# Kernel optimization log

Measured on AMD Instinct MI355X. Metric: run time of the kernel, lower is better.

## Reference

```python
import jax, jax.numpy as jnp
import numpy as np

B, S, D_IN, D_OUT = 4, 8192, 1024, 1024


def setup_inputs() -> dict:
    key = jax.random.key(0)
    k1, k2, k3, k4 = jax.random.split(key, 4)
    x = jax.random.normal(k1, (B, S, D_IN), dtype=jnp.float32)
    # signed int8 weights, stored int8 as in the torch buffer
    weight_int = jax.random.randint(k2, (D_OUT, D_IN), -128, 128, dtype=jnp.int32).astype(jnp.int8)
    # realistic per-output-channel scales
    weight_scale = jax.random.uniform(k3, (D_OUT,), dtype=jnp.float32, minval=0.005, maxval=0.02)
    input_scale = jnp.asarray(0.05, dtype=jnp.float32)
    bias = jax.random.normal(k4, (D_OUT,), dtype=jnp.float32) * 0.01
    return {"x": x, "weight_int": weight_int, "weight_scale": weight_scale,
            "input_scale": input_scale, "bias": bias}


def reference(x, weight_int, weight_scale, input_scale, bias):
    # quantize activations to int8 (faithful: round, clamp, cast)
    x_int = jnp.clip(jnp.round(x / input_scale), -128, 127).astype(jnp.int8)
    # module upcasts both operands to fp32 for the matmul
    out = jnp.matmul(x_int.astype(jnp.float32), weight_int.astype(jnp.float32).T)
    # dequantize: per-output-channel weight scale * scalar input scale, then bias
    out = out * weight_scale * input_scale + bias
    return out
```

## Files before the change

### kernel.cpp

```cpp
#include <hip/hip_runtime.h>
#include <stdint.h>
#include <stddef.h>

typedef int   v4i __attribute__((ext_vector_type(4)));
typedef float v4f __attribute__((ext_vector_type(4)));

#define BM 128
#define BN 128
#define BKB 128
#define M_DIM 32768
#define N_DIM 1024
#define K_DIM 1024

typedef const __attribute__((address_space(1))) void gvoid_t;
typedef __attribute__((address_space(3))) void lvoid_t;

__device__ __forceinline__ void gload16(const void* g, void* l) {
    __builtin_amdgcn_global_load_lds((gvoid_t*)g, (lvoid_t*)l, 16, 0, 0);
}

__global__ __launch_bounds__(256)
void repack_w_kernel(const int* __restrict__ wi, int* __restrict__ wq, int n4)
{
    int i = blockIdx.x * blockDim.x + threadIdx.x;
    if (i < n4) {
        v4i v = ((const v4i*)wi)[i];
        wq[i] = (v[0] & 255) | ((v[1] & 255) << 8) |
                ((v[2] & 255) << 16) | ((v[3] & 255) << 24);
    }
}

__global__ __launch_bounds__(256, 2)
void quant_kernel(const float* __restrict__ x, int* __restrict__ q,
                  const float* __restrict__ iscale_p, int n4)
{
    const float is = *iscale_p;
    int idx = blockIdx.x * blockDim.x + threadIdx.x;
    int stride = gridDim.x * blockDim.x;
    const v4f* xp = (const v4f*)x;
    for (int i = idx; i < n4; i += stride) {
        v4f v = xp[i];
        int r = 0;
        #pragma unroll
        for (int j = 0; j < 4; ++j) {
            float t = rintf(v[j] / is);
            t = fminf(127.f, fmaxf(-128.f, t));
            r |= ((int)t & 255) << (8 * j);
        }
        q[i] = r;
    }
}

__global__ __launch_bounds__(256, 2)
void qgemm_kernel(const signed char* __restrict__ Aq,
                  const signed char* __restrict__ W,
                  const float* __restrict__ wscale,
                  const float* __restrict__ iscale_p,
                  const float* __restrict__ bias,
                  float* __restrict__ out)
{
    __shared__ signed char lA[BM * BKB];
    __shared__ signed char lB[BN * BKB];

    const int nwg = gridDim.x;
    const int bid = blockIdx.x;
    const int wg  = (bid & 7) * (nwg >> 3) + (bid >> 3);
    const int m_blk = wg >> 3;
    const int n_blk = wg & 7;
    const int mrow0 = m_blk * BM;
    const int ncol0 = n_blk * BN;

    const int tid = threadIdx.x;
    const int wv  = tid >> 6;
    const int ln  = tid & 63;
    const int wm  = wv >> 1;
    const int wn  = wv & 1;
    const int lrow = ln & 15;
    const int lk16 = (ln >> 4) << 4;
    const int swz  = (lrow & 7) << 4;

    v4i acc[4][4] = {};

    for (int kt = 0; kt < K_DIM; kt += BKB) {
        __syncthreads();
        #pragma unroll
        for (int c = 0; c < 4; ++c) {
            const int o   = c * 4096 + wv * 1024 + ln * 16;
            const int row = o >> 7;
            const int inr = (o & 127) ^ ((row & 7) << 4);
            gload16(Aq + (size_t)(mrow0 + row) * K_DIM + kt + inr,
                    (void*)(lA + c * 4096 + wv * 1024));
            gload16(W + (size_t)(ncol0 + row) * K_DIM + kt + inr,
                    (void*)(lB + c * 4096 + wv * 1024));
        }
        __syncthreads();
        #pragma unroll
        for (int st = 0; st < 2; ++st) {
            v4i af[4], bf[4];
            #pragma unroll
            for (int i = 0; i < 4; ++i) {
                const int arow = wm * 64 + i * 16 + lrow;
                af[i] = *(const v4i*)&lA[arow * BKB + ((st * 64 + lk16) ^ swz)];
                const int brow = wn * 64 + i * 16 + lrow;
                bf[i] = *(const v4i*)&lB[brow * BKB + ((st * 64 + lk16) ^ swz)];
            }
            #pragma unroll
            for (int i = 0; i < 4; ++i)
                #pragma unroll
                for (int j = 0; j < 4; ++j)
                    acc[i][j] = __builtin_amdgcn_mfma_i32_16x16x64_i8(
                                    af[i], bf[j], acc[i][j], 0, 0, 0);
        }
    }

    const float is = *iscale_p;
    const int r0 = mrow0 + wm * 64 + ((ln >> 4) << 2);
    const int c0 = ncol0 + wn * 64 + lrow;
    #pragma unroll
    for (int j = 0; j < 4; ++j) {
        const int col = c0 + j * 16;
        const float sc = wscale[col] * is;
        const float bv = bias[col];
        #pragma unroll
        for (int i = 0; i < 4; ++i) {
            const int row = r0 + i * 16;
            #pragma unroll
            for (int r = 0; r < 4; ++r)
                out[(size_t)(row + r) * N_DIM + col] = (float)acc[i][j][r] * sc + bv;
        }
    }
}

extern "C" void kernel_launch(void* const* d_in, const int* in_sizes, int n_in,
                              void* d_out, int out_size, void* d_ws, size_t ws_size,
                              hipStream_t stream)
{
    const float* x       = (const float*)d_in[0];
    const int*   w32     = (const int*)d_in[1];
    const float* wscale  = (const float*)d_in[2];
    const float* iscale  = (const float*)d_in[3];
    const float* bias    = (const float*)d_in[4];
    float* out           = (float*)d_out;

    signed char* aq = (signed char*)d_ws;
    signed char* wq = (signed char*)d_ws + (size_t)M_DIM * K_DIM;

    const int wn4 = (N_DIM * K_DIM) / 4;
    repack_w_kernel<<<(wn4 + 255) / 256, 256, 0, stream>>>(w32, (int*)wq, wn4);

    quant_kernel<<<8192, 256, 0, stream>>>(x, (int*)aq, iscale, (M_DIM * K_DIM) / 4);

    const int grid = (M_DIM / BM) * (N_DIM / BN);
    qgemm_kernel<<<grid, 256, 0, stream>>>(aq, wq, wscale, iscale, bias, out);
}
```

Before: 85.49 us.

## Use 256x256 tiles with double-buffered LDS and interleaved load/MFMA pipeline

Rewrites the int8 GEMM to use 256x256 output tiles with 512 threads and double-buffered LDS. Global-to-LDS loads for the next K tile are split into quarters and interleaved between four MFMA phases, coordinated with explicit vmcnt waits, barriers and setprio. This raises arithmetic intensity and hides load latency, at the cost of more LDS (128KB) and more registers per thread, which may limit occupancy. The quantization kernel also replaces its per-element division with a multiply by a precomputed reciprocal, which can change rounding in rare cases.

```diff
diff --git a/kernel.cpp b/kernel.cpp
--- a/kernel.cpp
+++ b/kernel.cpp
@@ -5,12 +5,13 @@
 typedef int   v4i __attribute__((ext_vector_type(4)));
 typedef float v4f __attribute__((ext_vector_type(4)));
 
-#define BM 128
-#define BN 128
-#define BKB 128
 #define M_DIM 32768
 #define N_DIM 1024
 #define K_DIM 1024
+#define BM 256
+#define BN 256
+#define BK 128
+#define NT (K_DIM / BK)
 
 typedef const __attribute__((address_space(1))) void gvoid_t;
 typedef __attribute__((address_space(3))) void lvoid_t;
@@ -18,6 +19,10 @@
 __device__ __forceinline__ void gload16(const void* g, void* l) {
     __builtin_amdgcn_global_load_lds((gvoid_t*)g, (lvoid_t*)l, 16, 0, 0);
 }
+
+#define VMCNT(n)  asm volatile("s_waitcnt vmcnt(" #n ")" ::: "memory")
+#define BARRIER() do { asm volatile("s_barrier" ::: "memory"); \
+                       __builtin_amdgcn_sched_barrier(0); } while (0)
 
 __global__ __launch_bounds__(256)
 void repack_w_kernel(const int* __restrict__ wi, int* __restrict__ wq, int n4)
@@ -34,7 +39,7 @@
 void quant_kernel(const float* __restrict__ x, int* __restrict__ q,
                   const float* __restrict__ iscale_p, int n4)
 {
-    const float is = *iscale_p;
+    const float inv = 1.0f / *iscale_p;
     int idx = blockIdx.x * blockDim.x + threadIdx.x;
     int stride = gridDim.x * blockDim.x;
     const v4f* xp = (const v4f*)x;
@@ -43,7 +48,7 @@
         int r = 0;
         #pragma unroll
         for (int j = 0; j < 4; ++j) {
-            float t = rintf(v[j] / is);
+            float t = rintf(v[j] * inv);
             t = fminf(127.f, fmaxf(-128.f, t));
             r |= ((int)t & 255) << (8 * j);
         }
@@ -51,7 +56,35 @@
     }
 }
 
-__global__ __launch_bounds__(256, 2)
+__device__ __forceinline__ void stageA(const signed char* __restrict__ gA,
+                                       signed char* ldsA, int q, int wv, int ln)
+{
+    #pragma unroll
+    for (int l = 0; l < 2; ++l) {
+        const int r0  = l * 128 + q * 64 + wv * 8;
+        const int row = r0 + (ln >> 3);
+        const int col = ((ln & 7) * 16) ^ ((ln >> 3) << 4);
+        gload16(gA + (size_t)row * K_DIM + col, ldsA + r0 * BK);
+    }
+}
+__device__ __forceinline__ void stageB(const signed char* __restrict__ gB,
+                                       signed char* ldsB, int q, int wv, int ln)
+{
+    #pragma unroll
+    for (int l = 0; l < 2; ++l) {
+        const int r0  = (2 * l + (wv >> 2)) * 64 + q * 32 + (wv & 3) * 8;
+        const int row = r0 + (ln >> 3);
+        const int col = ((ln & 7) * 16) ^ ((ln >> 3) << 4);
+        gload16(gB + (size_t)row * K_DIM + col, ldsB + r0 * BK);
+    }
+}
+
+__device__ __forceinline__ v4i ldsRead(const signed char* lds, int row, int colb)
+{
+    return *(const v4i*)(lds + row * BK + (colb ^ ((row & 7) << 4)));
+}
+
+__global__ __launch_bounds__(512, 2)
 void qgemm_kernel(const signed char* __restrict__ Aq,
                   const signed char* __restrict__ W,
                   const float* __restrict__ wscale,
@@ -59,74 +92,137 @@
                   const float* __restrict__ bias,
                   float* __restrict__ out)
 {
-    __shared__ signed char lA[BM * BKB];
-    __shared__ signed char lB[BN * BKB];
-
-    const int nwg = gridDim.x;
+    __shared__ signed char lA[2][BM * BK];
+    __shared__ signed char lB[2][BN * BK];
+
     const int bid = blockIdx.x;
-    const int wg  = (bid & 7) * (nwg >> 3) + (bid >> 3);
-    const int m_blk = wg >> 3;
-    const int n_blk = wg & 7;
+    const int wg  = (bid & 7) * 64 + (bid >> 3);
+    const int m_blk = wg >> 2;
+    const int n_blk = wg & 3;
     const int mrow0 = m_blk * BM;
     const int ncol0 = n_blk * BN;
 
     const int tid = threadIdx.x;
     const int wv  = tid >> 6;
     const int ln  = tid & 63;
-    const int wm  = wv >> 1;
-    const int wn  = wv & 1;
-    const int lrow = ln & 15;
-    const int lk16 = (ln >> 4) << 4;
-    const int swz  = (lrow & 7) << 4;
-
-    v4i acc[4][4] = {};
-
-    for (int kt = 0; kt < K_DIM; kt += BKB) {
-        __syncthreads();
-        #pragma unroll
-        for (int c = 0; c < 4; ++c) {
-            const int o   = c * 4096 + wv * 1024 + ln * 16;
-            const int row = o >> 7;
-            const int inr = (o & 127) ^ ((row & 7) << 4);
-            gload16(Aq + (size_t)(mrow0 + row) * K_DIM + kt + inr,
-                    (void*)(lA + c * 4096 + wv * 1024));
-            gload16(W + (size_t)(ncol0 + row) * K_DIM + kt + inr,
-                    (void*)(lB + c * 4096 + wv * 1024));
-        }
-        __syncthreads();
-        #pragma unroll
-        for (int st = 0; st < 2; ++st) {
-            v4i af[4], bf[4];
-            #pragma unroll
-            for (int i = 0; i < 4; ++i) {
-                const int arow = wm * 64 + i * 16 + lrow;
-                af[i] = *(const v4i*)&lA[arow * BKB + ((st * 64 + lk16) ^ swz)];
-                const int brow = wn * 64 + i * 16 + lrow;
-                bf[i] = *(const v4i*)&lB[brow * BKB + ((st * 64 + lk16) ^ swz)];
-            }
-            #pragma unroll
-            for (int i = 0; i < 4; ++i)
-                #pragma unroll
-                for (int j = 0; j < 4; ++j)
-                    acc[i][j] = __builtin_amdgcn_mfma_i32_16x16x64_i8(
-                                    af[i], bf[j], acc[i][j], 0, 0, 0);
-        }
+    const int wm  = wv >> 2;
+    const int wn  = wv & 3;
+    const int lr  = ln & 15;
+    const int kc  = (ln >> 4) * 16;
+
+    const signed char* gA = Aq + (size_t)mrow0 * K_DIM;
+    const signed char* gB = W  + (size_t)ncol0 * K_DIM;
+
+    v4i acc[8][4] = {};
+    v4i aF[4][2];
+    v4i bF[2][2][2];
+
+    stageA(gA, lA[0], 0, wv, ln);
+    stageB(gB, lB[0], 0, wv, ln);
+    stageB(gB, lB[0], 1, wv, ln);
+    stageA(gA, lA[0], 1, wv, ln);
+
+    #pragma unroll
+    for (int t = 0; t < NT; ++t) {
+        const signed char* cA = lA[t & 1];
+        const signed char* cB = lB[t & 1];
+        signed char* nA = lA[(t + 1) & 1];
+        signed char* nB = lB[(t + 1) & 1];
+        const size_t ktn = (size_t)(t + 1) * BK;
+        const bool st = (t + 1 < NT);
+
+        VMCNT(4);
+        BARRIER();
+        #pragma unroll
+        for (int m = 0; m < 4; ++m)
+            #pragma unroll
+            for (int ks = 0; ks < 2; ++ks)
+                aF[m][ks] = ldsRead(cA, wm * 128 + m * 16 + lr, ks * 64 + kc);
+        #pragma unroll
+        for (int n = 0; n < 2; ++n)
+            #pragma unroll
+            for (int ks = 0; ks < 2; ++ks)
+                bF[0][n][ks] = ldsRead(cB, wn * 64 + n * 16 + lr, ks * 64 + kc);
+        if (st) stageA(gA + ktn, nA, 0, wv, ln);
+        BARRIER();
+        __builtin_amdgcn_s_setprio(1);
+        #pragma unroll
+        for (int m = 0; m < 4; ++m)
+            #pragma unroll
+            for (int n = 0; n < 2; ++n)
+                #pragma unroll
+                for (int ks = 0; ks < 2; ++ks)
+                    acc[m][n] = __builtin_amdgcn_mfma_i32_16x16x64_i8(
+                                    aF[m][ks], bF[0][n][ks], acc[m][n], 0, 0, 0);
+        __builtin_amdgcn_s_setprio(0);
+
+        if (st) { VMCNT(4); } else { VMCNT(2); }
+        BARRIER();
+        #pragma unroll
+        for (int n = 0; n < 2; ++n)
+            #pragma unroll
+            for (int ks = 0; ks < 2; ++ks)
+                bF[1][n][ks] = ldsRead(cB, wn * 64 + 32 + n * 16 + lr, ks * 64 + kc);
+        if (st) stageB(gB + ktn, nB, 0, wv, ln);
+        BARRIER();
+        __builtin_amdgcn_s_setprio(1);
+        #pragma unroll
+        for (int m = 0; m < 4; ++m)
+            #pragma unroll
+            for (int n = 0; n < 2; ++n)
+                #pragma unroll
+                for (int ks = 0; ks < 2; ++ks)
+                    acc[m][2 + n] = __builtin_amdgcn_mfma_i32_16x16x64_i8(
+                                    aF[m][ks], bF[1][n][ks], acc[m][2 + n], 0, 0, 0);
+        __builtin_amdgcn_s_setprio(0);
+
+        if (st) { VMCNT(4); } else { VMCNT(0); }
+        BARRIER();
+        #pragma unroll
+        for (int m = 0; m < 4; ++m)
+            #pragma unroll
+            for (int ks = 0; ks < 2; ++ks)
+                aF[m][ks] = ldsRead(cA, wm * 128 + 64 + m * 16 + lr, ks * 64 + kc);
+        if (st) stageB(gB + ktn, nB, 1, wv, ln);
+        BARRIER();
+        __builtin_amdgcn_s_setprio(1);
+        #pragma unroll
+        for (int m = 0; m < 4; ++m)
+            #pragma unroll
+            for (int n = 0; n < 2; ++n)
+                #pragma unroll
+                for (int ks = 0; ks < 2; ++ks)
+                    acc[4 + m][2 + n] = __builtin_amdgcn_mfma_i32_16x16x64_i8(
+                                    aF[m][ks], bF[1][n][ks], acc[4 + m][2 + n], 0, 0, 0);
+        __builtin_amdgcn_s_setprio(0);
+
+        BARRIER();
+        if (st) stageA(gA + ktn, nA, 1, wv, ln);
+        BARRIER();
+        __builtin_amdgcn_s_setprio(1);
+        #pragma unroll
+        for (int m = 0; m < 4; ++m)
+            #pragma unroll
+            for (int n = 0; n < 2; ++n)
+                #pragma unroll
+                for (int ks = 0; ks < 2; ++ks)
+                    acc[4 + m][n] = __builtin_amdgcn_mfma_i32_16x16x64_i8(
+                                    aF[m][ks], bF[0][n][ks], acc[4 + m][n], 0, 0, 0);
+        __builtin_amdgcn_s_setprio(0);
     }
 
     const float is = *iscale_p;
-    const int r0 = mrow0 + wm * 64 + ((ln >> 4) << 2);
-    const int c0 = ncol0 + wn * 64 + lrow;
-    #pragma unroll
-    for (int j = 0; j < 4; ++j) {
-        const int col = c0 + j * 16;
+    #pragma unroll
+    for (int n = 0; n < 4; ++n) {
+        const int col = ncol0 + wn * 64 + n * 16 + lr;
         const float sc = wscale[col] * is;
         const float bv = bias[col];
         #pragma unroll
-        for (int i = 0; i < 4; ++i) {
-            const int row = r0 + i * 16;
+        for (int m = 0; m < 8; ++m) {
+            const int row = mrow0 + wm * 128 + m * 16 + ((ln >> 4) << 2);
             #pragma unroll
             for (int r = 0; r < 4; ++r)
-                out[(size_t)(row + r) * N_DIM + col] = (float)acc[i][j][r] * sc + bv;
+                out[(size_t)(row + r) * N_DIM + col] = (float)acc[m][n][r] * sc + bv;
         }
     }
 }
@@ -151,5 +247,5 @@
     quant_kernel<<<8192, 256, 0, stream>>>(x, (int*)aq, iscale, (M_DIM * K_DIM) / 4);
 
     const int grid = (M_DIM / BM) * (N_DIM / BN);
-    qgemm_kernel<<<grid, 256, 0, stream>>>(aq, wq, wscale, iscale, bias, out);
-}
+    qgemm_kernel<<<grid, 512, 0, stream>>>(aq, wq, wscale, iscale, bias, out);
+}
```

After: 91.08 us. 6.5% more time.

## Enlarge GEMM tiles to 256x256, double-buffer LDS, switch to 32x32x32 int8 MFMA

Applied to the files above, without the earlier changes.

The int8 GEMM now uses 256x256 output tiles with BK=64, giving each wave a 128x128 sub-tile built from 32x32x32 i8 MFMAs with 16-wide accumulators. The LDS stage is double-buffered so the next K-slice loads while the current one computes, with explicit vmcnt waits, raw barriers and setprio around the MFMA block. The quantizer also replaces a per-element divide with a multiply by a precomputed reciprocal, which can change rounding at ties relative to the reference. The larger accumulator footprint raises register pressure and lowers occupancy (launch bounds no longer request two blocks per CU).

```diff
diff --git a/kernel.cpp b/kernel.cpp
--- a/kernel.cpp
+++ b/kernel.cpp
@@ -2,15 +2,17 @@
 #include <stdint.h>
 #include <stddef.h>
 
-typedef int   v4i __attribute__((ext_vector_type(4)));
-typedef float v4f __attribute__((ext_vector_type(4)));
+typedef int   v4i  __attribute__((ext_vector_type(4)));
+typedef int   v16i __attribute__((ext_vector_type(16)));
+typedef float v4f  __attribute__((ext_vector_type(4)));
 
-#define BM 128
-#define BN 128
-#define BKB 128
 #define M_DIM 32768
 #define N_DIM 1024
 #define K_DIM 1024
+#define BM 256
+#define BN 256
+#define BK 64
+#define NT (K_DIM / BK)
 
 typedef const __attribute__((address_space(1))) void gvoid_t;
 typedef __attribute__((address_space(3))) void lvoid_t;
@@ -18,6 +20,10 @@
 __device__ __forceinline__ void gload16(const void* g, void* l) {
     __builtin_amdgcn_global_load_lds((gvoid_t*)g, (lvoid_t*)l, 16, 0, 0);
 }
+
+#define VMCNT0()  asm volatile("s_waitcnt vmcnt(0)" ::: "memory")
+#define BARRIER() do { asm volatile("s_barrier" ::: "memory"); \
+                       __builtin_amdgcn_sched_barrier(0); } while (0)
 
 __global__ __launch_bounds__(256)
 void repack_w_kernel(const int* __restrict__ wi, int* __restrict__ wq, int n4)
@@ -34,7 +40,7 @@
 void quant_kernel(const float* __restrict__ x, int* __restrict__ q,
                   const float* __restrict__ iscale_p, int n4)
 {
-    const float is = *iscale_p;
+    const float inv = 1.0f / *iscale_p;
     int idx = blockIdx.x * blockDim.x + threadIdx.x;
     int stride = gridDim.x * blockDim.x;
     const v4f* xp = (const v4f*)x;
@@ -43,7 +49,7 @@
         int r = 0;
         #pragma unroll
         for (int j = 0; j < 4; ++j) {
-            float t = rintf(v[j] / is);
+            float t = rintf(v[j] * inv);
             t = fminf(127.f, fmaxf(-128.f, t));
             r |= ((int)t & 255) << (8 * j);
         }
@@ -51,7 +57,26 @@
     }
 }
 
-__global__ __launch_bounds__(256, 2)
+__device__ __forceinline__ int swz(int row) { return ((row >> 1) & 3) << 4; }
+
+__device__ __forceinline__ void stage64(const signed char* __restrict__ g,
+                                        signed char* lds, int wv, int ln)
+{
+    #pragma unroll
+    for (int j = 0; j < 4; ++j) {
+        const int rbase = j * 64 + wv * 16;
+        const int row   = rbase + (ln >> 2);
+        const int src   = ((ln & 3) * 16) ^ swz(row);
+        gload16(g + (size_t)row * K_DIM + src, lds + rbase * BK);
+    }
+}
+
+__device__ __forceinline__ v4i frag(const signed char* lds, int row, int kb)
+{
+    return *(const v4i*)(lds + row * BK + (kb ^ swz(row)));
+}
+
+__global__ __launch_bounds__(256)
 void qgemm_kernel(const signed char* __restrict__ Aq,
                   const signed char* __restrict__ W,
                   const float* __restrict__ wscale,
@@ -59,14 +84,13 @@
                   const float* __restrict__ bias,
                   float* __restrict__ out)
 {
-    __shared__ signed char lA[BM * BKB];
-    __shared__ signed char lB[BN * BKB];
+    __shared__ signed char lA[2][BM * BK];
+    __shared__ signed char lB[2][BN * BK];
 
-    const int nwg = gridDim.x;
     const int bid = blockIdx.x;
-    const int wg  = (bid & 7) * (nwg >> 3) + (bid >> 3);
-    const int m_blk = wg >> 3;
-    const int n_blk = wg & 7;
+    const int wg  = (bid & 7) * 64 + (bid >> 3);
+    const int m_blk = wg >> 2;
+    const int n_blk = wg & 3;
     const int mrow0 = m_blk * BM;
     const int ncol0 = n_blk * BN;
 
@@ -75,58 +99,65 @@
     const int ln  = tid & 63;
     const int wm  = wv >> 1;
     const int wn  = wv & 1;
-    const int lrow = ln & 15;
-    const int lk16 = (ln >> 4) << 4;
-    const int swz  = (lrow & 7) << 4;
+    const int lr  = ln & 31;
+    const int kh  = (ln >> 5) * 16;
 
-    v4i acc[4][4] = {};
+    const signed char* gA = Aq + (size_t)mrow0 * K_DIM;
+    const signed char* gB = W  + (size_t)ncol0 * K_DIM;
 
-    for (int kt = 0; kt < K_DIM; kt += BKB) {
-        __syncthreads();
+    v16i acc[4][4] = {};
+
+    stage64(gA, lA[0], wv, ln);
+    stage64(gB, lB[0], wv, ln);
+    VMCNT0();
+    BARRIER();
+
+    signed char *cA = lA[0], *cB = lB[0], *nA = lA[1], *nB = lB[1];
+
+    for (int t = 0; t < NT; ++t) {
+        const bool st = (t + 1 < NT);
+        if (st) {
+            stage64(gA + (size_t)(t + 1) * BK, nA, wv, ln);
+            stage64(gB + (size_t)(t + 1) * BK, nB, wv, ln);
+        }
         #pragma unroll
-        for (int c = 0; c < 4; ++c) {
-            const int o   = c * 4096 + wv * 1024 + ln * 16;
-            const int row = o >> 7;
-            const int inr = (o & 127) ^ ((row & 7) << 4);
-            gload16(Aq + (size_t)(mrow0 + row) * K_DIM + kt + inr,
-                    (void*)(lA + c * 4096 + wv * 1024));
-            gload16(W + (size_t)(ncol0 + row) * K_DIM + kt + inr,
-                    (void*)(lB + c * 4096 + wv * 1024));
-        }
-        __syncthreads();
-        #pragma unroll
-        for (int st = 0; st < 2; ++st) {
-            v4i af[4], bf[4];
+        for (int ks = 0; ks < 2; ++ks) {
+            v4i aF[4], bF[4];
             #pragma unroll
             for (int i = 0; i < 4; ++i) {
-                const int arow = wm * 64 + i * 16 + lrow;
-                af[i] = *(const v4i*)&lA[arow * BKB + ((st * 64 + lk16) ^ swz)];
-                const int brow = wn * 64 + i * 16 + lrow;
-                bf[i] = *(const v4i*)&lB[brow * BKB + ((st * 64 + lk16) ^ swz)];
+                aF[i] = frag(cA, wm * 128 + i * 32 + lr, ks * 32 + kh);
+                bF[i] = frag(cB, wn * 128 + i * 32 + lr, ks * 32 + kh);
             }
+            __builtin_amdgcn_s_setprio(1);
             #pragma unroll
             for (int i = 0; i < 4; ++i)
                 #pragma unroll
                 for (int j = 0; j < 4; ++j)
-                    acc[i][j] = __builtin_amdgcn_mfma_i32_16x16x64_i8(
-                                    af[i], bf[j], acc[i][j], 0, 0, 0);
+                    acc[i][j] = __builtin_amdgcn_mfma_i32_32x32x32_i8(
+                                    aF[i], bF[j], acc[i][j], 0, 0, 0);
+            __builtin_amdgcn_s_setprio(0);
         }
+        if (st) VMCNT0();
+        BARRIER();
+        signed char* s;
+        s = cA; cA = nA; nA = s;
+        s = cB; cB = nB; nB = s;
     }
 
     const float is = *iscale_p;
-    const int r0 = mrow0 + wm * 64 + ((ln >> 4) << 2);
-    const int c0 = ncol0 + wn * 64 + lrow;
     #pragma unroll
     for (int j = 0; j < 4; ++j) {
-        const int col = c0 + j * 16;
+        const int col = ncol0 + wn * 128 + j * 32 + lr;
         const float sc = wscale[col] * is;
         const float bv = bias[col];
         #pragma unroll
         for (int i = 0; i < 4; ++i) {
-            const int row = r0 + i * 16;
+            const int rbase = mrow0 + wm * 128 + i * 32 + 4 * (ln >> 5);
             #pragma unroll
-            for (int r = 0; r < 4; ++r)
-                out[(size_t)(row + r) * N_DIM + col] = (float)acc[i][j][r] * sc + bv;
+            for (int r = 0; r < 16; ++r) {
+                const int row = rbase + (r & 3) + 8 * (r >> 2);
+                out[(size_t)row * N_DIM + col] = (float)acc[i][j][r] * sc + bv;
+            }
         }
     }
 }
```

New measurement: 105.3 us. 23.1% more time.

## Double-buffer LDS in int8 GEMM and fuse quantize with weight repack

Applied to the files above, without the earlier changes.

The GEMM main loop now uses two LDS buffers, so the global-to-LDS loads for the next K tile are issued before the MFMAs on the current tile. This replaces the two barriers per iteration with a single vmcnt wait plus barrier, and wraps the MFMA block in s_setprio. The activation quantize kernel and the weight repack kernel are merged into one launch by splitting on block index, removing one kernel launch. The quantize step now multiplies by a precomputed reciprocal instead of dividing. That could change rounding at exact .5 ties relative to the reference, and doubling LDS per block may lower occupancy.

```diff
diff --git a/kernel.cpp b/kernel.cpp
--- a/kernel.cpp
+++ b/kernel.cpp
@@ -11,6 +11,10 @@
 #define M_DIM 32768
 #define N_DIM 1024
 #define K_DIM 1024
+#define NT (K_DIM / BKB)
+#define QN4 (M_DIM * K_DIM / 4)
+#define WN4 (N_DIM * K_DIM / 4)
+#define QBLOCKS 8192
 
 typedef const __attribute__((address_space(1))) void gvoid_t;
 typedef __attribute__((address_space(3))) void lvoid_t;
@@ -19,35 +23,39 @@
     __builtin_amdgcn_global_load_lds((gvoid_t*)g, (lvoid_t*)l, 16, 0, 0);
 }
 
+#define VMCNT0()  asm volatile("s_waitcnt vmcnt(0)" ::: "memory")
+#define BARRIER() do { asm volatile("s_barrier" ::: "memory"); \
+                       __builtin_amdgcn_sched_barrier(0); } while (0)
+
 __global__ __launch_bounds__(256)
-void repack_w_kernel(const int* __restrict__ wi, int* __restrict__ wq, int n4)
+void quant_repack_kernel(const float* __restrict__ x, int* __restrict__ q,
+                         const int* __restrict__ wi, int* __restrict__ wq,
+                         const float* __restrict__ iscale_p)
 {
-    int i = blockIdx.x * blockDim.x + threadIdx.x;
-    if (i < n4) {
-        v4i v = ((const v4i*)wi)[i];
-        wq[i] = (v[0] & 255) | ((v[1] & 255) << 8) |
-                ((v[2] & 255) << 16) | ((v[3] & 255) << 24);
-    }
-}
-
-__global__ __launch_bounds__(256, 2)
-void quant_kernel(const float* __restrict__ x, int* __restrict__ q,
-                  const float* __restrict__ iscale_p, int n4)
-{
-    const float is = *iscale_p;
-    int idx = blockIdx.x * blockDim.x + threadIdx.x;
-    int stride = gridDim.x * blockDim.x;
-    const v4f* xp = (const v4f*)x;
-    for (int i = idx; i < n4; i += stride) {
-        v4f v = xp[i];
-        int r = 0;
-        #pragma unroll
-        for (int j = 0; j < 4; ++j) {
-            float t = rintf(v[j] / is);
-            t = fminf(127.f, fmaxf(-128.f, t));
-            r |= ((int)t & 255) << (8 * j);
+    const int b = blockIdx.x;
+    if (b < QBLOCKS) {
+        const float inv = 1.0f / *iscale_p;
+        int idx = b * 256 + threadIdx.x;
+        const int stride = QBLOCKS * 256;
+        const v4f* xp = (const v4f*)x;
+        for (int i = idx; i < QN4; i += stride) {
+            v4f v = xp[i];
+            int r = 0;
+            #pragma unroll
+            for (int j = 0; j < 4; ++j) {
+                float t = rintf(v[j] * inv);
+                t = fminf(127.f, fmaxf(-128.f, t));
+                r |= ((int)t & 255) << (8 * j);
+            }
+            q[i] = r;
         }
-        q[i] = r;
+    } else {
+        const int i = (b - QBLOCKS) * 256 + threadIdx.x;
+        if (i < WN4) {
+            v4i v = ((const v4i*)wi)[i];
+            wq[i] = (v[0] & 255) | ((v[1] & 255) << 8) |
+                    ((v[2] & 255) << 16) | ((v[3] & 255) << 24);
+        }
     }
 }
 
@@ -59,8 +67,8 @@
                   const float* __restrict__ bias,
                   float* __restrict__ out)
 {
-    __shared__ signed char lA[BM * BKB];
-    __shared__ signed char lB[BN * BKB];
+    __shared__ signed char lA[2][BM * BKB];
+    __shared__ signed char lB[2][BN * BKB];
 
     const int nwg = gridDim.x;
     const int bid = blockIdx.x;
@@ -79,39 +87,59 @@
     const int lk16 = (ln >> 4) << 4;
     const int swz  = (lrow & 7) << 4;
 
+    const signed char* gA = Aq + (size_t)mrow0 * K_DIM;
+    const signed char* gB = W  + (size_t)ncol0 * K_DIM;
+
     v4i acc[4][4] = {};
 
-    for (int kt = 0; kt < K_DIM; kt += BKB) {
-        __syncthreads();
+    #define STAGE(buf, kt)                                                    \
+        do {                                                                  \
+            _Pragma("unroll")                                                 \
+            for (int c = 0; c < 4; ++c) {                                     \
+                const int o   = c * 4096 + wv * 1024 + ln * 16;               \
+                const int row = o >> 7;                                       \
+                const int inr = (o & 127) ^ ((row & 7) << 4);                 \
+                gload16(gA + (size_t)row * K_DIM + (kt) + inr,                \
+                        (void*)(lA[buf] + c * 4096 + wv * 1024));             \
+                gload16(gB + (size_t)row * K_DIM + (kt) + inr,                \
+                        (void*)(lB[buf] + c * 4096 + wv * 1024));             \
+            }                                                                 \
+        } while (0)
+
+    STAGE(0, 0);
+    VMCNT0();
+    BARRIER();
+
+    for (int t = 0; t < NT; ++t) {
+        const int cur = t & 1;
+        const bool st = (t + 1 < NT);
+        if (st) STAGE(cur ^ 1, (t + 1) * BKB);
+
+        const signed char* cA = lA[cur];
+        const signed char* cB = lB[cur];
         #pragma unroll
-        for (int c = 0; c < 4; ++c) {
-            const int o   = c * 4096 + wv * 1024 + ln * 16;
-            const int row = o >> 7;
-            const int inr = (o & 127) ^ ((row & 7) << 4);
-            gload16(Aq + (size_t)(mrow0 + row) * K_DIM + kt + inr,
-                    (void*)(lA + c * 4096 + wv * 1024));
-            gload16(W + (size_t)(ncol0 + row) * K_DIM + kt + inr,
-                    (void*)(lB + c * 4096 + wv * 1024));
-        }
-        __syncthreads();
-        #pragma unroll
-        for (int st = 0; st < 2; ++st) {
+        for (int stp = 0; stp < 2; ++stp) {
             v4i af[4], bf[4];
             #pragma unroll
             for (int i = 0; i < 4; ++i) {
                 const int arow = wm * 64 + i * 16 + lrow;
-                af[i] = *(const v4i*)&lA[arow * BKB + ((st * 64 + lk16) ^ swz)];
+                af[i] = *(const v4i*)&cA[arow * BKB + ((stp * 64 + lk16) ^ swz)];
                 const int brow = wn * 64 + i * 16 + lrow;
-                bf[i] = *(const v4i*)&lB[brow * BKB + ((st * 64 + lk16) ^ swz)];
+                bf[i] = *(const v4i*)&cB[brow * BKB + ((stp * 64 + lk16) ^ swz)];
             }
+            __builtin_amdgcn_s_setprio(1);
             #pragma unroll
             for (int i = 0; i < 4; ++i)
                 #pragma unroll
                 for (int j = 0; j < 4; ++j)
                     acc[i][j] = __builtin_amdgcn_mfma_i32_16x16x64_i8(
                                     af[i], bf[j], acc[i][j], 0, 0, 0);
+            __builtin_amdgcn_s_setprio(0);
         }
+        if (st) VMCNT0();
+        BARRIER();
     }
+    #undef STAGE
 
     const float is = *iscale_p;
     const int r0 = mrow0 + wm * 64 + ((ln >> 4) << 2);
@@ -145,10 +173,9 @@
     signed char* aq = (signed char*)d_ws;
     signed char* wq = (signed char*)d_ws + (size_t)M_DIM * K_DIM;
 
-    const int wn4 = (N_DIM * K_DIM) / 4;
-    repack_w_kernel<<<(wn4 + 255) / 256, 256, 0, stream>>>(w32, (int*)wq, wn4);
-
-    quant_kernel<<<8192, 256, 0, stream>>>(x, (int*)aq, iscale, (M_DIM * K_DIM) / 4);
+    const int wblocks = (WN4 + 255) / 256;
+    quant_repack_kernel<<<QBLOCKS + wblocks, 256, 0, stream>>>(
+        x, (int*)aq, w32, (int*)wq, iscale);
 
     const int grid = (M_DIM / BM) * (N_DIM / BN);
     qgemm_kernel<<<grid, 256, 0, stream>>>(aq, wq, wscale, iscale, bias, out);
```

New measurement: 85.32 us. No clear change (-0.2%).
